# Optimization experiments

Measured on AMD Instinct MI355X. Metric: run time of the kernel, lower is better.

## Reference

```python
import jax, jax.numpy as jnp
import numpy as np

H = 192  # GRU hidden size


def gru_bidir_layer(x, w_ih, w_hh, b_ih, b_hh):
    # x: [B,T,Din]; w_ih: [2,3H,Din]; w_hh: [2,3H,H]; b_ih/b_hh: [2,3H]
    # PyTorch GRU gate order: r, z, n
    B = x.shape[0]

    def run_dir(d, reverse):
        gx = jnp.einsum('btd,gd->btg', x, w_ih[d]) + b_ih[d]  # [B,T,3H] input gates, precomputed
        gx = jnp.swapaxes(gx, 0, 1)  # [T,B,3H]
        h0 = jnp.zeros((B, H), x.dtype)

        def step(h, g):
            gh = h @ w_hh[d].T + b_hh[d]  # [B,3H]
            r = jax.nn.sigmoid(g[:, :H] + gh[:, :H])
            z = jax.nn.sigmoid(g[:, H:2 * H] + gh[:, H:2 * H])
            n = jnp.tanh(g[:, 2 * H:] + r * gh[:, 2 * H:])
            h_new = (1.0 - z) * n + z * h
            return h_new, h_new

        _, hs = jax.lax.scan(step, h0, gx, reverse=reverse)
        return jnp.swapaxes(hs, 0, 1)  # [B,T,H], time-ordered

    return jnp.concatenate([run_dir(0, False), run_dir(1, True)], axis=-1)  # [B,T,2H]


def setup_inputs() -> dict:
    key = jax.random.key(0)
    ks = jax.random.split(key, 20)
    B, T, V, E = 128, 512, 120000, 128
    s = 1.0 / np.sqrt(H)
    x = jax.random.randint(ks[0], (B, T), 0, V)
    emb = jax.random.normal(ks[1], (V, E), jnp.float32) * 0.05
    emb = emb.at[0].set(0.0)  # padding_idx=0
    d = {'x': x, 'emb': emb}
    din = [E, 2 * H, 2 * H]
    for l in range(3):
        d[f'w_ih{l}'] = jax.random.uniform(ks[2 + 4 * l], (2, 3 * H, din[l]), jnp.float32, -s, s)
        d[f'w_hh{l}'] = jax.random.uniform(ks[3 + 4 * l], (2, 3 * H, H), jnp.float32, -s, s)
        d[f'b_ih{l}'] = jax.random.uniform(ks[4 + 4 * l], (2, 3 * H), jnp.float32, -s, s)
        d[f'b_hh{l}'] = jax.random.uniform(ks[5 + 4 * l], (2, 3 * H), jnp.float32, -s, s)
    d['fc1_w'] = jax.random.uniform(ks[14], (128, 2 * H), jnp.float32, -s, s)
    d['fc1_b'] = jax.random.uniform(ks[15], (128,), jnp.float32, -s, s)
    d['fc2_w'] = jax.random.uniform(ks[16], (1, 128), jnp.float32, -s, s)
    d['fc2_b'] = jax.random.uniform(ks[17], (1,), jnp.float32, -s, s)
    return d


def reference(x, emb, w_ih0, w_hh0, b_ih0, b_hh0, w_ih1, w_hh1, b_ih1, b_hh1,
              w_ih2, w_hh2, b_ih2, b_hh2, fc1_w, fc1_b, fc2_w, fc2_b):
    h = emb[x]  # [B,T,128]
    h = gru_bidir_layer(h, w_ih0, w_hh0, b_ih0, b_hh0)
    h = gru_bidir_layer(h, w_ih1, w_hh1, b_ih1, b_hh1)  # inter-layer dropout is identity at inference
    h = gru_bidir_layer(h, w_ih2, w_hh2, b_ih2, b_hh2)
    y = h[:, -1, :]  # last timestep, [B, 384]
    y = jax.nn.relu(y @ fc1_w.T + fc1_b)
    y = y @ fc2_w.T + fc2_b  # [B,1]
    return y[:, 0]
```

## Files before the change

### kernel.cpp

```cpp
#include <hip/hip_runtime.h>

typedef _Float16 f16;
typedef _Float16 f16x8 __attribute__((ext_vector_type(8)));
typedef _Float16 f16x4 __attribute__((ext_vector_type(4)));
typedef _Float16 f16x2 __attribute__((ext_vector_type(2)));
typedef float f32x4 __attribute__((ext_vector_type(4)));

#define B_ 128
#define T_ 512
#define H_ 192
#define G3 576

#define SC_RZ (-1.44269504088896f)
#define SC_N  (2.88539008177793f)

#define OFF_H   150994944u
#define OFF_WIH 201326592u
#define OFF_WHH 203390976u

__device__ __forceinline__ void gload_lds16(const void* g, void* l) {
  __builtin_amdgcn_global_load_lds(
      (const __attribute__((address_space(1))) unsigned int*)g,
      (__attribute__((address_space(3))) unsigned int*)l, 16, 0, 0);
}

__global__ void wconv_kernel(const float* __restrict__ w0, const float* __restrict__ h0,
                             const float* __restrict__ w1, const float* __restrict__ h1,
                             const float* __restrict__ w2, const float* __restrict__ h2,
                             f16* __restrict__ wih, f16* __restrict__ whh) {
  const int stride = gridDim.x * blockDim.x;
  for (int i = blockIdx.x * blockDim.x + threadIdx.x; i < 1695744; i += stride) {
    if (i < 1032192) {
      int j, din;
      const float* src;
      if (i < 147456) { j = i; din = 128; src = w0; }
      else if (i < 589824) { j = i - 147456; din = 384; src = w1; }
      else { j = i - 589824; din = 384; src = w2; }
      const int row = j / din;
      const int sg = (row % 576) / 192;
      wih[i] = (f16)(src[j] * (sg == 2 ? SC_N : SC_RZ));
    } else {
      int j = i - 1032192, jl;
      const float* src;
      if (j < 221184) { src = h0; jl = j; }
      else if (j < 442368) { src = h1; jl = j - 221184; }
      else { src = h2; jl = j - 442368; }
      const int row = jl / 192;
      const int sg = (row % 576) / 192;
      whh[j] = (f16)(src[jl] * (sg == 2 ? SC_N : SC_RZ));
    }
  }
}

__global__ void embed_kernel(const int* __restrict__ x, const float* __restrict__ emb,
                             f16* __restrict__ o) {
  const int row = (blockIdx.x << 2) + (threadIdx.x >> 6);
  const int lane = threadIdx.x & 63;
  const int b = row >> 9, t = row & 511;
  const int idx = x[row];
  const float2 v = *(const float2*)(emb + ((size_t)idx << 7) + (lane << 1));
  union { f16 h[2]; unsigned u; } p;
  p.h[0] = (f16)v.x;
  p.h[1] = (f16)v.y;
  *(unsigned*)(o + ((size_t)((t << 7) + b) << 7) + (lane << 1)) = p.u;
}

template <int DIN>
__global__ __launch_bounds__(256) void gx_gemm(const f16* __restrict__ A,
                                               const f16* __restrict__ W,
                                               const float* __restrict__ bih,
                                               f16* __restrict__ gxo) {
  const int t = blockIdx.x;
  const int nt0 = blockIdx.y << 7;
  const int tid = threadIdx.x;
  const int lane = tid & 63;
  const int w = tid >> 6;
  const int l16 = lane & 15;
  const int lq = lane >> 4;
  const int wm = (w >> 1) << 6;
  const int wn = (w & 1) << 6;

  __shared__ __align__(16) f16 Al[128 * 128];
  __shared__ __align__(16) f16 Bl[128 * 128];

  f32x4 acc[4][4] = {};

  const int srow = tid >> 4;
  const int sc = tid & 15;

  for (int kk = 0; kk < DIN; kk += 128) {
    __syncthreads();
#pragma unroll
    for (int it = 0; it < 8; ++it) {
      const int r = (it << 4) + srow;
      const int cl = sc ^ (r & 7);
      gload_lds16(A + (size_t)(t * B_ + r) * DIN + kk + cl * 8, Al + (it << 11) + tid * 8);
      const int n = nt0 + r;
      gload_lds16(W + (size_t)n * DIN + kk + cl * 8, Bl + (it << 11) + tid * 8);
    }
    __syncthreads();
#pragma unroll
    for (int kt = 0; kt < 4; ++kt) {
      f16x8 af[4], bf[4];
#pragma unroll
      for (int mt = 0; mt < 4; ++mt) {
        const int r = wm + (mt << 4) + l16;
        const int c = ((kt << 2) + lq) ^ (r & 7);
        af[mt] = *(const f16x8*)(Al + (r << 7) + (c << 3));
      }
#pragma unroll
      for (int nt = 0; nt < 4; ++nt) {
        const int r = wn + (nt << 4) + l16;
        const int c = ((kt << 2) + lq) ^ (r & 7);
        bf[nt] = *(const f16x8*)(Bl + (r << 7) + (c << 3));
      }
#pragma unroll
      for (int mt = 0; mt < 4; ++mt)
#pragma unroll
        for (int nt = 0; nt < 4; ++nt)
          acc[mt][nt] = __builtin_amdgcn_mfma_f32_16x16x32_f16(af[mt], bf[nt], acc[mt][nt], 0, 0, 0);
    }
  }
#pragma unroll
  for (int nt = 0; nt < 4; ++nt) {
    const int ncol = nt0 + wn + (nt << 4);
    const int ntile = ncol >> 4;
    const int dd = (ntile >= 36) ? 1 : 0;
    const int g = ntile - 36 * dd;
    const int s = g / 12;
    const int c12 = g % 12;
    const float bias = bih[ncol + l16] * ((s == 2) ? SC_N : SC_RZ);
#pragma unroll
    for (int mt = 0; mt < 4; ++mt) {
      const int bblk16 = (wm >> 4) + mt;
      const int bblk8 = bblk16 * 2 + (lq >> 1);
      f16x2 p0, p1;
      p0[0] = (f16)(acc[mt][nt][0] + bias);
      p0[1] = (f16)(acc[mt][nt][1] + bias);
      p1[0] = (f16)(acc[mt][nt][2] + bias);
      p1[1] = (f16)(acc[mt][nt][3] + bias);
      const size_t base =
          ((((size_t)(dd * 16 + bblk8) * 512 + t) * 12 + c12) * 4 + (lq & 1)) * 96 +
          l16 * 6 + s * 2;
      *(f16x2*)(gxo + base) = p0;
      *(f16x2*)(gxo + base + 192) = p1;
    }
  }
}

__global__ __launch_bounds__(768, 3) void gru_scan(const f16* __restrict__ gx,
                                                   const f16* __restrict__ whh,
                                                   const float* __restrict__ bhh,
                                                   f16* __restrict__ out,
                                                   int last) {
  const int bx = blockIdx.x;
  const int d = bx & 1;
  const int bblk8 = bx >> 1;
  const int b0 = bblk8 << 3;
  const int tid = threadIdx.x;
  const int lane = tid & 63;
  const int w = tid >> 6;
  const int l16 = lane & 15;
  const int lq = lane >> 4;

  __shared__ __align__(16) f16 hl[2 * 8 * 192];
  for (int i = tid; i < 2 * 8 * 192; i += 768) hl[i] = (f16)0.f;
  char* cb = (char*)hl;

  int ra[6];
#pragma unroll
  for (int kt = 0; kt < 6; ++kt)
    ra[kt] = (l16 & 7) * 384 + ((kt * 64 + lq * 16) ^ ((l16 & 7) << 4));
  const int r0 = ((lq & 1) << 2) | (lq & 2);
  const int cix = (w * 16 + l16) * 2;
  const int wa0 = r0 * 384 + (cix ^ (r0 << 4));
  const int wa1 = (r0 + 1) * 384 + (cix ^ ((r0 + 1) << 4));
  const bool hi = (lq & 2) != 0;

  const f16* whd = whh + (size_t)d * (G3 * H_);
  f16x8 wf[3][6];
#pragma unroll
  for (int s = 0; s < 3; ++s) {
    const int nrow = s * 192 + w * 16 + l16;
#pragma unroll
    for (int kt = 0; kt < 6; ++kt)
      wf[s][kt] = *(const f16x8*)(whd + (size_t)nrow * H_ + kt * 32 + lq * 8);
  }
  f32x4 bh4[3];
#pragma unroll
  for (int s = 0; s < 3; ++s) {
    const float bv = bhh[d * G3 + s * 192 + w * 16 + l16] * ((s == 2) ? SC_N : SC_RZ);
    bh4[s] = (f32x4){bv, bv, bv, bv};
  }

  float hr0 = 0.f, hr1 = 0.f;

  const int nsteps = (last && d == 1) ? 1 : T_;
  const bool fwd = (d == 0);
  const long gstep = fwd ? 4608 : -4608;
  const long ostep = fwd ? (long)B_ * 384 : -(long)B_ * 384;
  const int t0 = fwd ? 0 : (T_ - 1);

  const f16* gbase = gx + (size_t)(d * 16 + bblk8) * 2359296 +
                     (size_t)(((w * 4 + lq) * 16 + l16) * 6);

  auto ld3 = [](const f16* p, f16x2 (&g)[3]) {
    g[0] = *(const f16x2*)(p);
    g[1] = *(const f16x2*)(p + 2);
    g[2] = *(const f16x2*)(p + 4);
  };

  f16x2 pA[3] = {}, pB[3] = {};
  ld3(gbase + (size_t)t0 * 4608, pA);
  if (nsteps > 1) ld3(gbase + (size_t)t0 * 4608 + gstep, pB);
  const f16* gptr = gbase + (size_t)t0 * 4608 + 2 * gstep;
  f16* outp = out + ((size_t)t0 * B_ + b0 + r0) * 384 + d * H_ + w * 16 + l16;

  __syncthreads();

  auto body = [&](int step, int buf, f16x2 (&pc)[3]) {
    const int bo = buf ? 3072 : 0;
    const f16x2 g0 = pc[0], g1 = pc[1], g2 = pc[2];
    if (step + 2 < nsteps) {
      ld3(gptr, pc);
      gptr += gstep;
    }
    f32x4 acc[3];
    {
      const f16x8 af0 = *(const f16x8*)(cb + ra[0] + bo);
#pragma unroll
      for (int s = 0; s < 3; ++s)
        acc[s] = __builtin_amdgcn_mfma_f32_16x16x32_f16(af0, wf[s][0], bh4[s], 0, 0, 0);
    }
#pragma unroll
    for (int kt = 1; kt < 6; ++kt) {
      const f16x8 af = *(const f16x8*)(cb + ra[kt] + bo);
#pragma unroll
      for (int s = 0; s < 3; ++s)
        acc[s] = __builtin_amdgcn_mfma_f32_16x16x32_f16(af, wf[s][kt], acc[s], 0, 0, 0);
    }
    const int t = fwd ? step : (T_ - 1 - step);
    const bool wr = (!last) || (t == T_ - 1);
    const int bo2 = buf ? 0 : 3072;
    const float a0r = hi ? acc[0][2] : acc[0][0];
    const float a0z = hi ? acc[1][2] : acc[1][0];
    const float a0n = hi ? acc[2][2] : acc[2][0];
    const float a1r = hi ? acc[0][3] : acc[0][1];
    const float a1z = hi ? acc[1][3] : acc[1][1];
    const float a1n = hi ? acc[2][3] : acc[2][1];
    {
      const float ur = (float)g0[0] + a0r;
      const float uz = (float)g1[0] + a0z;
      const float dr = 1.f + __builtin_amdgcn_exp2f(ur);
      const float dz = 1.f + __builtin_amdgcn_exp2f(uz);
      const float Rp = __builtin_amdgcn_rcpf(dr * dz);
      const float rv = dz * Rp, zv = dr * Rp;
      const float vn = fmaf(rv, a0n, (float)g2[0]);
      const float nv = fmaf(-2.f, __builtin_amdgcn_rcpf(1.f + __builtin_amdgcn_exp2f(vn)), 1.f);
      const float hv = nv + zv * (hr0 - nv);
      hr0 = hv;
      *(f16*)(cb + wa0 + bo2) = (f16)hv;
      if (wr) outp[0] = (f16)hv;
    }
    {
      const float ur = (float)g0[1] + a1r;
      const float uz = (float)g1[1] + a1z;
      const float dr = 1.f + __builtin_amdgcn_exp2f(ur);
      const float dz = 1.f + __builtin_amdgcn_exp2f(uz);
      const float Rp = __builtin_amdgcn_rcpf(dr * dz);
      const float rv = dz * Rp, zv = dr * Rp;
      const float vn = fmaf(rv, a1n, (float)g2[1]);
      const float nv = fmaf(-2.f, __builtin_amdgcn_rcpf(1.f + __builtin_amdgcn_exp2f(vn)), 1.f);
      const float hv = nv + zv * (hr1 - nv);
      hr1 = hv;
      *(f16*)(cb + wa1 + bo2) = (f16)hv;
      if (wr) outp[384] = (f16)hv;
    }
    outp += ostep;
    __syncthreads();
  };

  if (nsteps == 1) {
    body(0, 0, pA);
  } else {
    for (int step = 0; step < T_; step += 2) {
      body(step, 0, pA);
      body(step + 1, 1, pB);
    }
  }
}

__global__ void fc_kernel(const f16* __restrict__ h2, const float* __restrict__ w1,
                          const float* __restrict__ b1, const float* __restrict__ w2,
                          const float* __restrict__ b2, float* __restrict__ y) {
  const int b = blockIdx.x;
  const int i = threadIdx.x;
  __shared__ float hs[384];
  __shared__ float us[128];
  const f16* hp = h2 + ((size_t)(T_ - 1) * B_ + b) * 384;
  for (int k = i; k < 384; k += 128) hs[k] = (float)hp[k];
  __syncthreads();
  float a = b1[i];
  for (int k = 0; k < 384; ++k) a = fmaf(w1[i * 384 + k], hs[k], a);
  us[i] = fmaxf(a, 0.f) * w2[i];
  __syncthreads();
  if (i == 0) {
    float s = b2[0];
    for (int k = 0; k < 128; ++k) s += us[k];
    y[b] = s;
  }
}

extern "C" void kernel_launch(void* const* d_in, const int* in_sizes, int n_in,
                              void* d_out, int out_size, void* d_ws, size_t ws_size,
                              hipStream_t stream) {
  const int* x = (const int*)d_in[0];
  const float* emb = (const float*)d_in[1];
  const float* wih[3] = {(const float*)d_in[2], (const float*)d_in[6], (const float*)d_in[10]};
  const float* whh[3] = {(const float*)d_in[3], (const float*)d_in[7], (const float*)d_in[11]};
  const float* bih[3] = {(const float*)d_in[4], (const float*)d_in[8], (const float*)d_in[12]};
  const float* bhh[3] = {(const float*)d_in[5], (const float*)d_in[9], (const float*)d_in[13]};
  const float* fc1w = (const float*)d_in[14];
  const float* fc1b = (const float*)d_in[15];
  const float* fc2w = (const float*)d_in[16];
  const float* fc2b = (const float*)d_in[17];
  float* y = (float*)d_out;

  char* ws = (char*)d_ws;
  f16* gxb = (f16*)(ws);
  f16* hbuf = (f16*)(ws + OFF_H);
  f16* in0 = hbuf;
  f16* wihf = (f16*)(ws + OFF_WIH);
  f16* whhf = (f16*)(ws + OFF_WHH);

  wconv_kernel<<<1024, 256, 0, stream>>>(wih[0], whh[0], wih[1], whh[1], wih[2], whh[2], wihf, whhf);
  embed_kernel<<<16384, 256, 0, stream>>>(x, emb, in0);

  gx_gemm<128><<<dim3(512, 9), 256, 0, stream>>>(in0, wihf, bih[0], gxb);
  gru_scan<<<32, 768, 0, stream>>>(gxb, whhf, bhh[0], hbuf, 0);
  gx_gemm<384><<<dim3(512, 9), 256, 0, stream>>>(hbuf, wihf + 147456, bih[1], gxb);
  gru_scan<<<32, 768, 0, stream>>>(gxb, whhf + 221184, bhh[1], hbuf, 0);
  gx_gemm<384><<<dim3(512, 9), 256, 0, stream>>>(hbuf, wihf + 147456 + 442368, bih[2], gxb);
  gru_scan<<<32, 768, 0, stream>>>(gxb, whhf + 2 * 221184, bhh[2], hbuf, 1);

  fc_kernel<<<128, 128, 0, stream>>>(hbuf, fc1w, fc1b, fc2w, fc2b, y);
}
```

Baseline: 1.544 ms.

## Split GRU scan into 4-row batch blocks and launch 64 workgroups

Each scan workgroup now handles 4 batch rows instead of 8, so the launch doubles to 64 workgroups across the 128 batch rows and both directions. Each thread computes one hidden element per step instead of two, which shortens the serial per-step gate math. The LDS hidden-state buffer is halved and the gx gather indexing is remapped to the unchanged gx layout. The cost is that the MFMA tiles sit half-empty (16 rows with only 4 valid), the recurrent weights are loaded by twice as many workgroups, and the gx loads become scalar f16 reads.

After: 1.855 ms. 20.1% more time.

```diff
diff --git a/kernel.cpp b/kernel.cpp
--- a/kernel.cpp
+++ b/kernel.cpp
@@ -155,27 +155,24 @@
                                                    int last) {
   const int bx = blockIdx.x;
   const int d = bx & 1;
-  const int bblk8 = bx >> 1;
-  const int b0 = bblk8 << 3;
+  const int bblk4 = bx >> 1;
+  const int b0 = bblk4 << 2;
   const int tid = threadIdx.x;
   const int lane = tid & 63;
   const int w = tid >> 6;
   const int l16 = lane & 15;
   const int lq = lane >> 4;
 
-  __shared__ __align__(16) f16 hl[2 * 8 * 192];
-  for (int i = tid; i < 2 * 8 * 192; i += 768) hl[i] = (f16)0.f;
+  __shared__ __align__(16) f16 hl[2 * 4 * 192];
+  for (int i = tid; i < 2 * 4 * 192; i += 768) hl[i] = (f16)0.f;
   char* cb = (char*)hl;
 
   int ra[6];
 #pragma unroll
   for (int kt = 0; kt < 6; ++kt)
-    ra[kt] = (l16 & 7) * 384 + ((kt * 64 + lq * 16) ^ ((l16 & 7) << 4));
-  const int r0 = ((lq & 1) << 2) | (lq & 2);
+    ra[kt] = (l16 & 3) * 384 + ((kt * 64 + lq * 16) ^ ((l16 & 3) << 4));
   const int cix = (w * 16 + l16) * 2;
-  const int wa0 = r0 * 384 + (cix ^ (r0 << 4));
-  const int wa1 = (r0 + 1) * 384 + (cix ^ ((r0 + 1) << 4));
-  const bool hi = (lq & 2) != 0;
+  const int wa = lq * 384 + (cix ^ (lq << 4));
 
   const f16* whd = whh + (size_t)d * (G3 * H_);
   f16x8 wf[3][6];
@@ -193,7 +190,7 @@
     bh4[s] = (f32x4){bv, bv, bv, bv};
   }
 
-  float hr0 = 0.f, hr1 = 0.f;
+  float hr = 0.f;
 
   const int nsteps = (last && d == 1) ? 1 : T_;
   const bool fwd = (d == 0);
@@ -201,28 +198,31 @@
   const long ostep = fwd ? (long)B_ * 384 : -(long)B_ * 384;
   const int t0 = fwd ? 0 : (T_ - 1);
 
-  const f16* gbase = gx + (size_t)(d * 16 + bblk8) * 2359296 +
-                     (size_t)(((w * 4 + lq) * 16 + l16) * 6);
-
-  auto ld3 = [](const f16* p, f16x2 (&g)[3]) {
-    g[0] = *(const f16x2*)(p);
-    g[1] = *(const f16x2*)(p + 2);
-    g[2] = *(const f16x2*)(p + 4);
-  };
-
-  f16x2 pA[3] = {}, pB[3] = {};
-  ld3(gbase + (size_t)t0 * 4608, pA);
-  if (nsteps > 1) ld3(gbase + (size_t)t0 * 4608 + gstep, pB);
+  const int prow = ((bblk4 & 1) << 2) | lq;
+  const int lq_s = ((prow & 4) >> 2) | (prow & 2);
+  const int pair = prow & 1;
+  const f16* gbase = gx + (size_t)(d * 16 + (bblk4 >> 1)) * 2359296 +
+                     (size_t)(w * 384 + lq_s * 96 + l16 * 6 + pair);
+
+  f16 pA[3] = {}, pB[3] = {};
+  {
+    const f16* p = gbase + (size_t)t0 * 4608;
+    pA[0] = p[0]; pA[1] = p[2]; pA[2] = p[4];
+  }
+  if (nsteps > 1) {
+    const f16* p = gbase + (size_t)t0 * 4608 + gstep;
+    pB[0] = p[0]; pB[1] = p[2]; pB[2] = p[4];
+  }
   const f16* gptr = gbase + (size_t)t0 * 4608 + 2 * gstep;
-  f16* outp = out + ((size_t)t0 * B_ + b0 + r0) * 384 + d * H_ + w * 16 + l16;
+  f16* outp = out + ((size_t)t0 * B_ + b0 + lq) * 384 + d * H_ + w * 16 + l16;
 
   __syncthreads();
 
-  auto body = [&](int step, int buf, f16x2 (&pc)[3]) {
-    const int bo = buf ? 3072 : 0;
-    const f16x2 g0 = pc[0], g1 = pc[1], g2 = pc[2];
+  auto body = [&](int step, int buf, f16 (&pc)[3]) {
+    const int bo = buf ? 1536 : 0;
+    const f16 g0 = pc[0], g1 = pc[1], g2 = pc[2];
     if (step + 2 < nsteps) {
-      ld3(gptr, pc);
+      pc[0] = gptr[0]; pc[1] = gptr[2]; pc[2] = gptr[4];
       gptr += gstep;
     }
     f32x4 acc[3];
@@ -241,40 +241,24 @@
     }
     const int t = fwd ? step : (T_ - 1 - step);
     const bool wr = (!last) || (t == T_ - 1);
-    const int bo2 = buf ? 0 : 3072;
-    const float a0r = hi ? acc[0][2] : acc[0][0];
-    const float a0z = hi ? acc[1][2] : acc[1][0];
-    const float a0n = hi ? acc[2][2] : acc[2][0];
-    const float a1r = hi ? acc[0][3] : acc[0][1];
-    const float a1z = hi ? acc[1][3] : acc[1][1];
-    const float a1n = hi ? acc[2][3] : acc[2][1];
+    const int bo2 = buf ? 0 : 1536;
+    const bool s2 = (lq & 2) != 0, s1 = (lq & 1) != 0;
+    const float ar = s2 ? (s1 ? acc[0][3] : acc[0][2]) : (s1 ? acc[0][1] : acc[0][0]);
+    const float az = s2 ? (s1 ? acc[1][3] : acc[1][2]) : (s1 ? acc[1][1] : acc[1][0]);
+    const float an = s2 ? (s1 ? acc[2][3] : acc[2][2]) : (s1 ? acc[2][1] : acc[2][0]);
     {
-      const float ur = (float)g0[0] + a0r;
-      const float uz = (float)g1[0] + a0z;
+      const float ur = (float)g0 + ar;
+      const float uz = (float)g1 + az;
       const float dr = 1.f + __builtin_amdgcn_exp2f(ur);
       const float dz = 1.f + __builtin_amdgcn_exp2f(uz);
       const float Rp = __builtin_amdgcn_rcpf(dr * dz);
       const float rv = dz * Rp, zv = dr * Rp;
-      const float vn = fmaf(rv, a0n, (float)g2[0]);
+      const float vn = fmaf(rv, an, (float)g2);
       const float nv = fmaf(-2.f, __builtin_amdgcn_rcpf(1.f + __builtin_amdgcn_exp2f(vn)), 1.f);
-      const float hv = nv + zv * (hr0 - nv);
-      hr0 = hv;
-      *(f16*)(cb + wa0 + bo2) = (f16)hv;
-      if (wr) outp[0] = (f16)hv;
-    }
-    {
-      const float ur = (float)g0[1] + a1r;
-      const float uz = (float)g1[1] + a1z;
-      const float dr = 1.f + __builtin_amdgcn_exp2f(ur);
-      const float dz = 1.f + __builtin_amdgcn_exp2f(uz);
-      const float Rp = __builtin_amdgcn_rcpf(dr * dz);
-      const float rv = dz * Rp, zv = dr * Rp;
-      const float vn = fmaf(rv, a1n, (float)g2[1]);
-      const float nv = fmaf(-2.f, __builtin_amdgcn_rcpf(1.f + __builtin_amdgcn_exp2f(vn)), 1.f);
-      const float hv = nv + zv * (hr1 - nv);
-      hr1 = hv;
-      *(f16*)(cb + wa1 + bo2) = (f16)hv;
-      if (wr) outp[384] = (f16)hv;
+      const float hv = nv + zv * (hr - nv);
+      hr = hv;
+      *(f16*)(cb + wa + bo2) = (f16)hv;
+      if (wr) *outp = (f16)hv;
     }
     outp += ostep;
     __syncthreads();
@@ -337,11 +321,11 @@
   embed_kernel<<<16384, 256, 0, stream>>>(x, emb, in0);
 
   gx_gemm<128><<<dim3(512, 9), 256, 0, stream>>>(in0, wihf, bih[0], gxb);
-  gru_scan<<<32, 768, 0, stream>>>(gxb, whhf, bhh[0], hbuf, 0);
+  gru_scan<<<64, 768, 0, stream>>>(gxb, whhf, bhh[0], hbuf, 0);
   gx_gemm<384><<<dim3(512, 9), 256, 0, stream>>>(hbuf, wihf + 147456, bih[1], gxb);
-  gru_scan<<<32, 768, 0, stream>>>(gxb, whhf + 221184, bhh[1], hbuf, 0);
+  gru_scan<<<64, 768, 0, stream>>>(gxb, whhf + 221184, bhh[1], hbuf, 0);
   gx_gemm<384><<<dim3(512, 9), 256, 0, stream>>>(hbuf, wihf + 147456 + 442368, bih[2], gxb);
-  gru_scan<<<32, 768, 0, stream>>>(gxb, whhf + 2 * 221184, bhh[2], hbuf, 1);
+  gru_scan<<<64, 768, 0, stream>>>(gxb, whhf + 2 * 221184, bhh[2], hbuf, 1);
 
   fc_kernel<<<128, 128, 0, stream>>>(hbuf, fc1w, fc1b, fc2w, fc2b, y);
 }
```

## Fuse prep kernels, skip unused reverse-direction gates in last layer, batch scan output stores

Applied to the files above, without the earlier changes.

Merges the embedding gather and weight conversion into one launch. In the last layer the input-gate GEMM skips reverse-direction tiles for all but the final timestep, because only the last output timestep is consumed and the backward scan needs just one step there. The scan kernel now buffers four steps of hidden output in registers and writes them out together. It also moves the next gate prefetch after the MFMA chain. This cuts launches, GEMM work and per-step global stores, at the cost of extra registers and more complex control flow.

Measured after the change: 1.427 ms. 1.08x faster.

```diff
diff --git a/kernel.cpp b/kernel.cpp
--- a/kernel.cpp
+++ b/kernel.cpp
@@ -24,12 +24,26 @@
       (__attribute__((address_space(3))) unsigned int*)l, 16, 0, 0);
 }
 
-__global__ void wconv_kernel(const float* __restrict__ w0, const float* __restrict__ h0,
-                             const float* __restrict__ w1, const float* __restrict__ h1,
-                             const float* __restrict__ w2, const float* __restrict__ h2,
-                             f16* __restrict__ wih, f16* __restrict__ whh) {
-  const int stride = gridDim.x * blockDim.x;
-  for (int i = blockIdx.x * blockDim.x + threadIdx.x; i < 1695744; i += stride) {
+__global__ void prep_kernel(const int* __restrict__ x, const float* __restrict__ emb,
+                            f16* __restrict__ o,
+                            const float* __restrict__ w0, const float* __restrict__ h0,
+                            const float* __restrict__ w1, const float* __restrict__ h1,
+                            const float* __restrict__ w2, const float* __restrict__ h2,
+                            f16* __restrict__ wih, f16* __restrict__ whh) {
+  if (blockIdx.x < 16384) {
+    const int row = (blockIdx.x << 2) + (threadIdx.x >> 6);
+    const int lane = threadIdx.x & 63;
+    const int b = row >> 9, t = row & 511;
+    const int idx = x[row];
+    const float2 v = *(const float2*)(emb + ((size_t)idx << 7) + (lane << 1));
+    union { f16 h[2]; unsigned u; } p;
+    p.h[0] = (f16)v.x;
+    p.h[1] = (f16)v.y;
+    *(unsigned*)(o + ((size_t)((t << 7) + b) << 7) + (lane << 1)) = p.u;
+    return;
+  }
+  const int bid = blockIdx.x - 16384;
+  for (int i = bid * blockDim.x + threadIdx.x; i < 1695744; i += 1024 * 256) {
     if (i < 1032192) {
       int j, din;
       const float* src;
@@ -52,26 +66,15 @@
   }
 }
 
-__global__ void embed_kernel(const int* __restrict__ x, const float* __restrict__ emb,
-                             f16* __restrict__ o) {
-  const int row = (blockIdx.x << 2) + (threadIdx.x >> 6);
-  const int lane = threadIdx.x & 63;
-  const int b = row >> 9, t = row & 511;
-  const int idx = x[row];
-  const float2 v = *(const float2*)(emb + ((size_t)idx << 7) + (lane << 1));
-  union { f16 h[2]; unsigned u; } p;
-  p.h[0] = (f16)v.x;
-  p.h[1] = (f16)v.y;
-  *(unsigned*)(o + ((size_t)((t << 7) + b) << 7) + (lane << 1)) = p.u;
-}
-
 template <int DIN>
 __global__ __launch_bounds__(256) void gx_gemm(const f16* __restrict__ A,
                                                const f16* __restrict__ W,
                                                const float* __restrict__ bih,
-                                               f16* __restrict__ gxo) {
+                                               f16* __restrict__ gxo,
+                                               int lastmode) {
   const int t = blockIdx.x;
   const int nt0 = blockIdx.y << 7;
+  if (lastmode && nt0 >= 640 && t != 511) return;
   const int tid = threadIdx.x;
   const int lane = tid & 63;
   const int w = tid >> 6;
@@ -126,6 +129,7 @@
     const int ncol = nt0 + wn + (nt << 4);
     const int ntile = ncol >> 4;
     const int dd = (ntile >= 36) ? 1 : 0;
+    if (lastmode && dd == 1 && t != 511) continue;
     const int g = ntile - 36 * dd;
     const int s = g / 12;
     const int c12 = g % 12;
@@ -216,31 +220,37 @@
   const f16* gptr = gbase + (size_t)t0 * 4608 + 2 * gstep;
   f16* outp = out + ((size_t)t0 * B_ + b0 + r0) * 384 + d * H_ + w * 16 + l16;
 
+  f16x2 hist0 = {}, hist1 = {}, hist2 = {}, hist3 = {};
   __syncthreads();
 
-  auto body = [&](int step, int buf, f16x2 (&pc)[3]) {
+  auto flush4 = [&]() {
+    f16* p0 = outp - 4 * ostep; p0[0] = hist0[0]; p0[384] = hist0[1];
+    f16* p1 = outp - 3 * ostep; p1[0] = hist1[0]; p1[384] = hist1[1];
+    f16* p2 = outp - 2 * ostep; p2[0] = hist2[0]; p2[384] = hist2[1];
+    f16* p3 = outp - 1 * ostep; p3[0] = hist3[0]; p3[384] = hist3[1];
+  };
+
+  auto body = [&](int step, int buf, f16x2 (&pc)[3], const int ph) {
     const int bo = buf ? 3072 : 0;
+    f32x4 acc[3];
+    {
+      const f16x8 af0 = *(const f16x8*)(cb + ra[0] + bo);
+#pragma unroll
+      for (int s = 0; s < 3; ++s)
+        acc[s] = __builtin_amdgcn_mfma_f32_16x16x32_f16(af0, wf[s][0], bh4[s], 0, 0, 0);
+    }
+#pragma unroll
+    for (int kt = 1; kt < 6; ++kt) {
+      const f16x8 af = *(const f16x8*)(cb + ra[kt] + bo);
+#pragma unroll
+      for (int s = 0; s < 3; ++s)
+        acc[s] = __builtin_amdgcn_mfma_f32_16x16x32_f16(af, wf[s][kt], acc[s], 0, 0, 0);
+    }
     const f16x2 g0 = pc[0], g1 = pc[1], g2 = pc[2];
     if (step + 2 < nsteps) {
       ld3(gptr, pc);
       gptr += gstep;
     }
-    f32x4 acc[3];
-    {
-      const f16x8 af0 = *(const f16x8*)(cb + ra[0] + bo);
-#pragma unroll
-      for (int s = 0; s < 3; ++s)
-        acc[s] = __builtin_amdgcn_mfma_f32_16x16x32_f16(af0, wf[s][0], bh4[s], 0, 0, 0);
-    }
-#pragma unroll
-    for (int kt = 1; kt < 6; ++kt) {
-      const f16x8 af = *(const f16x8*)(cb + ra[kt] + bo);
-#pragma unroll
-      for (int s = 0; s < 3; ++s)
-        acc[s] = __builtin_amdgcn_mfma_f32_16x16x32_f16(af, wf[s][kt], acc[s], 0, 0, 0);
-    }
-    const int t = fwd ? step : (T_ - 1 - step);
-    const bool wr = (!last) || (t == T_ - 1);
     const int bo2 = buf ? 0 : 3072;
     const float a0r = hi ? acc[0][2] : acc[0][0];
     const float a0z = hi ? acc[1][2] : acc[1][0];
@@ -248,6 +258,7 @@
     const float a1r = hi ? acc[0][3] : acc[0][1];
     const float a1z = hi ? acc[1][3] : acc[1][1];
     const float a1n = hi ? acc[2][3] : acc[2][1];
+    f16x2 hcur;
     {
       const float ur = (float)g0[0] + a0r;
       const float uz = (float)g1[0] + a0z;
@@ -260,7 +271,7 @@
       const float hv = nv + zv * (hr0 - nv);
       hr0 = hv;
       *(f16*)(cb + wa0 + bo2) = (f16)hv;
-      if (wr) outp[0] = (f16)hv;
+      hcur[0] = (f16)hv;
     }
     {
       const float ur = (float)g0[1] + a1r;
@@ -274,19 +285,32 @@
       const float hv = nv + zv * (hr1 - nv);
       hr1 = hv;
       *(f16*)(cb + wa1 + bo2) = (f16)hv;
-      if (wr) outp[384] = (f16)hv;
+      hcur[1] = (f16)hv;
+    }
+    if (!last) {
+      if (ph == 0) hist0 = hcur;
+      else if (ph == 1) hist1 = hcur;
+      else if (ph == 2) hist2 = hcur;
+      else hist3 = hcur;
+    } else {
+      const int t = fwd ? step : (T_ - 1 - step);
+      if (t == T_ - 1) { outp[0] = hcur[0]; outp[384] = hcur[1]; }
     }
     outp += ostep;
     __syncthreads();
   };
 
   if (nsteps == 1) {
-    body(0, 0, pA);
+    body(0, 0, pA, 0);
   } else {
-    for (int step = 0; step < T_; step += 2) {
-      body(step, 0, pA);
-      body(step + 1, 1, pB);
-    }
+    for (int step = 0; step < T_; step += 4) {
+      if (!last && step > 0) flush4();
+      body(step + 0, 0, pA, 0);
+      body(step + 1, 1, pB, 1);
+      body(step + 2, 0, pA, 2);
+      body(step + 3, 1, pB, 3);
+    }
+    if (!last) flush4();
   }
 }
 
@@ -333,14 +357,14 @@
   f16* wihf = (f16*)(ws + OFF_WIH);
   f16* whhf = (f16*)(ws + OFF_WHH);
 
-  wconv_kernel<<<1024, 256, 0, stream>>>(wih[0], whh[0], wih[1], whh[1], wih[2], whh[2], wihf, whhf);
-  embed_kernel<<<16384, 256, 0, stream>>>(x, emb, in0);
-
-  gx_gemm<128><<<dim3(512, 9), 256, 0, stream>>>(in0, wihf, bih[0], gxb);
+  prep_kernel<<<17408, 256, 0, stream>>>(x, emb, in0, wih[0], whh[0], wih[1], whh[1],
+                                         wih[2], whh[2], wihf, whhf);
+
+  gx_gemm<128><<<dim3(512, 9), 256, 0, stream>>>(in0, wihf, bih[0], gxb, 0);
   gru_scan<<<32, 768, 0, stream>>>(gxb, whhf, bhh[0], hbuf, 0);
-  gx_gemm<384><<<dim3(512, 9), 256, 0, stream>>>(hbuf, wihf + 147456, bih[1], gxb);
+  gx_gemm<384><<<dim3(512, 9), 256, 0, stream>>>(hbuf, wihf + 147456, bih[1], gxb, 0);
   gru_scan<<<32, 768, 0, stream>>>(gxb, whhf + 221184, bhh[1], hbuf, 0);
-  gx_gemm<384><<<dim3(512, 9), 256, 0, stream>>>(hbuf, wihf + 147456 + 442368, bih[2], gxb);
+  gx_gemm<384><<<dim3(512, 9), 256, 0, stream>>>(hbuf, wihf + 147456 + 442368, bih[2], gxb, 1);
   gru_scan<<<32, 768, 0, stream>>>(gxb, whhf + 2 * 221184, bhh[2], hbuf, 1);
 
   fc_kernel<<<128, 128, 0, stream>>>(hbuf, fc1w, fc1b, fc2w, fc2b, y);
```
